# Kernel optimization log

Measured on AMD Instinct MI355X. Metric: run time of the kernel, lower is better.

Reference implementation:

```python
import jax, jax.numpy as jnp
import numpy as np
from jax import lax

KSIZE = 11
SIGMA = 1.5
C1 = (0.01 * 1.0) ** 2
C2 = (0.03 * 1.0) ** 2
PAD = (KSIZE - 1) // 2  # 5


def _gaussian_2d(ksize: int, sigma: float) -> np.ndarray:
    half = (ksize - 1) * 0.5
    g = np.exp(-0.5 * (np.linspace(-half, half, ksize) / sigma) ** 2)
    g = g / g.sum()
    return np.outer(g, g).astype(np.float32)  # [k, k]


def setup_inputs() -> dict:
    key = jax.random.key(0)
    kx, ky = jax.random.split(key)
    B, C, T, H, W = 2, 3, 8, 512, 512
    x = jax.random.uniform(kx, (B, C, T, H, W), dtype=jnp.float32)
    y = jax.random.uniform(ky, (B, C, T, H, W), dtype=jnp.float32)
    k2d = jnp.asarray(_gaussian_2d(KSIZE, SIGMA))
    # depthwise conv3d kernel: [C_out=C, C_in/groups=1, kD=1, kH, kW]
    kernel = jnp.broadcast_to(k2d[None, None, None], (C, 1, 1, KSIZE, KSIZE))
    return {"x": x, "y": y, "kernel": kernel}


def reference(x, y, kernel):
    C = x.shape[1]

    def conv(z):
        return lax.conv_general_dilated(
            z, kernel,
            window_strides=(1, 1, 1),
            padding=((0, 0), (PAD, PAD), (PAD, PAD)),
            dimension_numbers=("NCDHW", "OIDHW", "NCDHW"),
            feature_group_count=C,
        )

    # single grouped conv over the 5 stacked statistics, as in the original
    stacked = jnp.concatenate([x, y, x * x, y * y, x * y], axis=0)
    ux, uy, uxx, uyy, uxy = jnp.split(conv(stacked), 5, axis=0)

    vx = uxx - ux * ux
    vy = uyy - uy * uy
    vxy = uxy - ux * uy
    a1 = 2.0 * ux * uy + C1
    a2 = 2.0 * vxy + C2
    b1 = ux * ux + uy * uy + C1
    b2 = vx + vy + C2
    return a1 * a2 / (b1 * b2)
```

## Files before the change

kernel.cpp:

```cpp
#include <hip/hip_runtime.h>
#include <type_traits>

namespace {
constexpr int HH = 512;
constexpr int WW = 512;
constexpr int KS = 11;
constexpr int PADR = 5;
constexpr int TH = 32;
constexpr int TW = 64;
constexpr int SLAB = 16;
constexpr int HC = TW + 2 * PADR;
constexpr int LP = 80;
constexpr int NTHREADS = 256;
constexpr float SSIM_C1 = 1.0e-4f;
constexpr float SSIM_C2 = 9.0e-4f;
}

__global__ __launch_bounds__(NTHREADS, 4) void ssim_fused(
    const float* __restrict__ x, const float* __restrict__ y,
    const float* __restrict__ kern, float* __restrict__ out)
{
    __shared__ float vb[5][SLAB][LP];

    constexpr int tiles_w = WW / TW;
    constexpr int tiles_h = HH / TH;
    constexpr int tpp = tiles_w * tiles_h;

    const int bid = blockIdx.x;
    const int plane = bid / tpp;
    const int trem = bid - plane * tpp;
    const int tr_idx = trem / tiles_w;
    const int tile_r = tr_idx * TH;
    const int tile_c = (trem - tr_idx * tiles_w) * TW;

    const float* __restrict__ xp = x + (size_t)plane * (HH * WW);
    const float* __restrict__ yp = y + (size_t)plane * (HH * WW);
    float* __restrict__ op = out + (size_t)plane * (HH * WW);

    float wt[KS];
    {
        const float c = kern[5 * KS + 5];
        const float inv = rsqrtf(c);
#pragma unroll
        for (int i = 0; i < KS; ++i) wt[i] = kern[5 * KS + i] * inv;
    }

    const int t = threadIdx.x;
    const bool interior = (tile_r >= PADR) && (tile_r + TH + PADR <= HH) &&
                          (tile_c >= PADR) && (tile_c + TW + PADR <= WW);

    const int p2_r = t >> 4;
    const int p2_c0 = (t & 15) * 4;

    auto run_slab = [&](int s0, auto intr_tag) {
        constexpr bool INTR = decltype(intr_tag)::value;
        for (int i = t; i < (SLAB / 2) * HC; i += NTHREADS) {
            const int r2 = i / HC;
            const int c = i - r2 * HC;
            const int gr = tile_r + s0 + 2 * r2;
            const int gc = tile_c + c - PADR;
            float sxA = 0.f, syA = 0.f, sxxA = 0.f, syyA = 0.f, sxyA = 0.f;
            float sxB = 0.f, syB = 0.f, sxxB = 0.f, syyB = 0.f, sxyB = 0.f;
            if (INTR) {
                const float* xq = xp + (gr - PADR) * WW + gc;
                const float* yq = yp + (gr - PADR) * WW + gc;
#pragma unroll
                for (int k = 0; k < KS + 1; ++k) {
                    const float xv = xq[k * WW];
                    const float yv = yq[k * WW];
                    const float xx = xv * xv;
                    const float yy = yv * yv;
                    const float xy = xv * yv;
                    if (k < KS) {
                        const float w = wt[k];
                        sxA += w * xv;  syA += w * yv;
                        sxxA += w * xx; syyA += w * yy; sxyA += w * xy;
                    }
                    if (k >= 1) {
                        const float w = wt[k - 1];
                        sxB += w * xv;  syB += w * yv;
                        sxxB += w * xx; syyB += w * yy; sxyB += w * xy;
                    }
                }
            } else {
                const bool cok = (gc >= 0) & (gc < WW);
#pragma unroll
                for (int k = 0; k < KS + 1; ++k) {
                    const int rr = gr - PADR + k;
                    const bool ok = cok & (rr >= 0) & (rr < HH);
                    float xv = 0.f, yv = 0.f;
                    if (ok) {
                        xv = xp[rr * WW + gc];
                        yv = yp[rr * WW + gc];
                    }
                    const float xx = xv * xv;
                    const float yy = yv * yv;
                    const float xy = xv * yv;
                    if (k < KS) {
                        const float w = wt[k];
                        sxA += w * xv;  syA += w * yv;
                        sxxA += w * xx; syyA += w * yy; sxyA += w * xy;
                    }
                    if (k >= 1) {
                        const float w = wt[k - 1];
                        sxB += w * xv;  syB += w * yv;
                        sxxB += w * xx; syyB += w * yy; sxyB += w * xy;
                    }
                }
            }
            const int rA = 2 * r2, rB = 2 * r2 + 1;
            vb[0][rA][c] = sxA;   vb[0][rB][c] = sxB;
            vb[1][rA][c] = syA;   vb[1][rB][c] = syB;
            vb[2][rA][c] = sxxA;  vb[2][rB][c] = sxxB;
            vb[3][rA][c] = syyA;  vb[3][rB][c] = syyB;
            vb[4][rA][c] = sxyA;  vb[4][rB][c] = sxyB;
        }
        __syncthreads();

        float res[5][4];
#pragma unroll
        for (int s = 0; s < 5; ++s) {
            const float4 q0 = *(const float4*)&vb[s][p2_r][p2_c0];
            const float4 q1 = *(const float4*)&vb[s][p2_r][p2_c0 + 4];
            const float4 q2 = *(const float4*)&vb[s][p2_r][p2_c0 + 8];
            const float4 q3 = *(const float4*)&vb[s][p2_r][p2_c0 + 12];
            float wnd[16] = {q0.x, q0.y, q0.z, q0.w,
                             q1.x, q1.y, q1.z, q1.w,
                             q2.x, q2.y, q2.z, q2.w,
                             q3.x, q3.y, q3.z, q3.w};
#pragma unroll
            for (int j = 0; j < 4; ++j) {
                float a = 0.f;
#pragma unroll
                for (int k = 0; k < KS; ++k) a += wt[k] * wnd[j + k];
                res[s][j] = a;
            }
        }
        float4 o4;
#pragma unroll
        for (int j = 0; j < 4; ++j) {
            const float ux = res[0][j], uy = res[1][j];
            const float uxx = res[2][j], uyy = res[3][j], uxy = res[4][j];
            const float vx  = uxx - ux * ux;
            const float vy  = uyy - uy * uy;
            const float vxy = uxy - ux * uy;
            const float a1 = 2.f * ux * uy + SSIM_C1;
            const float a2 = 2.f * vxy + SSIM_C2;
            const float b1 = ux * ux + uy * uy + SSIM_C1;
            const float b2 = vx + vy + SSIM_C2;
            (&o4.x)[j] = (a1 * a2) * __builtin_amdgcn_rcpf(b1 * b2);
        }
        *(float4*)(op + (size_t)(tile_r + s0 + p2_r) * WW + (tile_c + p2_c0)) = o4;
        __syncthreads();
    };

    if (interior) {
        run_slab(0,    std::true_type{});
        run_slab(SLAB, std::true_type{});
    } else {
        run_slab(0,    std::false_type{});
        run_slab(SLAB, std::false_type{});
    }
}

extern "C" void kernel_launch(void* const* d_in, const int* in_sizes, int n_in,
                              void* d_out, int out_size, void* d_ws, size_t ws_size,
                              hipStream_t stream) {
    const float* x    = (const float*)d_in[0];
    const float* y    = (const float*)d_in[1];
    const float* kern = (const float*)d_in[2];
    float* out = (float*)d_out;

    const int nplanes = in_sizes[0] / (HH * WW);
    const int nblocks = nplanes * (HH / TH) * (WW / TW);

    ssim_fused<<<dim3(nblocks), dim3(NTHREADS), 0, stream>>>(x, y, kern, out);
}
```

Before: 212.5 us.

## Pack x/y statistics into float2 pairs for packed FMA and interleaved LDS layout

```diff
diff --git a/kernel.cpp b/kernel.cpp
--- a/kernel.cpp
+++ b/kernel.cpp
@@ -10,17 +10,25 @@
 constexpr int TW = 64;
 constexpr int SLAB = 16;
 constexpr int HC = TW + 2 * PADR;
-constexpr int LP = 80;
+constexpr int LPA = 148;
+constexpr int LPC = 76;
 constexpr int NTHREADS = 256;
 constexpr float SSIM_C1 = 1.0e-4f;
 constexpr float SSIM_C2 = 9.0e-4f;
 }
 
+typedef float v2f __attribute__((ext_vector_type(2)));
+typedef float v4f __attribute__((ext_vector_type(4)));
+#define LOWP(v)  __builtin_shufflevector(v, v, 0, 1)
+#define HIGHP(v) __builtin_shufflevector(v, v, 2, 3)
+
 __global__ __launch_bounds__(NTHREADS, 4) void ssim_fused(
     const float* __restrict__ x, const float* __restrict__ y,
     const float* __restrict__ kern, float* __restrict__ out)
 {
-    __shared__ float vb[5][SLAB][LP];
+    __shared__ __align__(16) float pA[SLAB][LPA];
+    __shared__ __align__(16) float pB_[SLAB][LPA];
+    __shared__ __align__(16) float pC_[SLAB][LPC];
 
     constexpr int tiles_w = WW / TW;
     constexpr int tiles_h = HH / TH;
@@ -37,12 +45,15 @@
     const float* __restrict__ yp = y + (size_t)plane * (HH * WW);
     float* __restrict__ op = out + (size_t)plane * (HH * WW);
 
-    float wt[KS];
+    v2f pw[6];
     {
-        const float c = kern[5 * KS + 5];
-        const float inv = rsqrtf(c);
+        const float inv = rsqrtf(kern[5 * KS + 5]);
 #pragma unroll
-        for (int i = 0; i < KS; ++i) wt[i] = kern[5 * KS + i] * inv;
+        for (int i = 0; i < 6; ++i) {
+            const float w = kern[5 * KS + i] * inv;
+            v2f tmp = {w, w};
+            pw[i] = tmp;
+        }
     }
 
     const int t = threadIdx.x;
@@ -50,7 +61,7 @@
                           (tile_c >= PADR) && (tile_c + TW + PADR <= WW);
 
     const int p2_r = t >> 4;
-    const int p2_c0 = (t & 15) * 4;
+    const int p2_m = t & 15;
 
     auto run_slab = [&](int s0, auto intr_tag) {
         constexpr bool INTR = decltype(intr_tag)::value;
@@ -59,99 +70,134 @@
             const int c = i - r2 * HC;
             const int gr = tile_r + s0 + 2 * r2;
             const int gc = tile_c + c - PADR;
-            float sxA = 0.f, syA = 0.f, sxxA = 0.f, syyA = 0.f, sxyA = 0.f;
-            float sxB = 0.f, syB = 0.f, sxxB = 0.f, syyB = 0.f, sxyB = 0.f;
-            if (INTR) {
-                const float* xq = xp + (gr - PADR) * WW + gc;
-                const float* yq = yp + (gr - PADR) * WW + gc;
+            v2f uvA = {0.f, 0.f}, qqA = {0.f, 0.f};
+            v2f uvB = {0.f, 0.f}, qqB = {0.f, 0.f};
+            float xyA = 0.f, xyB = 0.f;
+            const float* xq = xp + (gr - PADR) * WW + gc;
+            const float* yq = yp + (gr - PADR) * WW + gc;
 #pragma unroll
-                for (int k = 0; k < KS + 1; ++k) {
-                    const float xv = xq[k * WW];
-                    const float yv = yq[k * WW];
-                    const float xx = xv * xv;
-                    const float yy = yv * yv;
-                    const float xy = xv * yv;
-                    if (k < KS) {
-                        const float w = wt[k];
-                        sxA += w * xv;  syA += w * yv;
-                        sxxA += w * xx; syyA += w * yy; sxyA += w * xy;
-                    }
-                    if (k >= 1) {
-                        const float w = wt[k - 1];
-                        sxB += w * xv;  syB += w * yv;
-                        sxxB += w * xx; syyB += w * yy; sxyB += w * xy;
-                    }
-                }
-            } else {
-                const bool cok = (gc >= 0) & (gc < WW);
-#pragma unroll
-                for (int k = 0; k < KS + 1; ++k) {
+            for (int k = 0; k < KS + 1; ++k) {
+                float xv, yv;
+                if (INTR) {
+                    xv = xq[k * WW];
+                    yv = yq[k * WW];
+                } else {
                     const int rr = gr - PADR + k;
-                    const bool ok = cok & (rr >= 0) & (rr < HH);
-                    float xv = 0.f, yv = 0.f;
+                    const bool ok = (gc >= 0) & (gc < WW) & (rr >= 0) & (rr < HH);
+                    xv = 0.f; yv = 0.f;
                     if (ok) {
                         xv = xp[rr * WW + gc];
                         yv = yp[rr * WW + gc];
                     }
-                    const float xx = xv * xv;
-                    const float yy = yv * yv;
-                    const float xy = xv * yv;
-                    if (k < KS) {
-                        const float w = wt[k];
-                        sxA += w * xv;  syA += w * yv;
-                        sxxA += w * xx; syyA += w * yy; sxyA += w * xy;
-                    }
-                    if (k >= 1) {
-                        const float w = wt[k - 1];
-                        sxB += w * xv;  syB += w * yv;
-                        sxxB += w * xx; syyB += w * yy; sxyB += w * xy;
-                    }
+                }
+                v2f v2 = {xv, yv};
+                const v2f q2 = v2 * v2;
+                const float xy = xv * yv;
+                if (k < KS) {
+                    const v2f w = pw[k < 6 ? k : 10 - k];
+                    uvA += w * v2;
+                    qqA += w * q2;
+                    xyA += w.x * xy;
+                }
+                if (k >= 1) {
+                    const v2f w = pw[(k - 1) < 6 ? (k - 1) : 11 - k];
+                    uvB += w * v2;
+                    qqB += w * q2;
+                    xyB += w.x * xy;
                 }
             }
             const int rA = 2 * r2, rB = 2 * r2 + 1;
-            vb[0][rA][c] = sxA;   vb[0][rB][c] = sxB;
-            vb[1][rA][c] = syA;   vb[1][rB][c] = syB;
-            vb[2][rA][c] = sxxA;  vb[2][rB][c] = sxxB;
-            vb[3][rA][c] = syyA;  vb[3][rB][c] = syyB;
-            vb[4][rA][c] = sxyA;  vb[4][rB][c] = sxyB;
+            *(v2f*)&pA[rA][2 * c] = uvA;   *(v2f*)&pA[rB][2 * c] = uvB;
+            *(v2f*)&pB_[rA][2 * c] = qqA;  *(v2f*)&pB_[rB][2 * c] = qqB;
+            pC_[rA][c] = xyA;              pC_[rB][c] = xyB;
         }
         __syncthreads();
 
-        float res[5][4];
-#pragma unroll
-        for (int s = 0; s < 5; ++s) {
-            const float4 q0 = *(const float4*)&vb[s][p2_r][p2_c0];
-            const float4 q1 = *(const float4*)&vb[s][p2_r][p2_c0 + 4];
-            const float4 q2 = *(const float4*)&vb[s][p2_r][p2_c0 + 8];
-            const float4 q3 = *(const float4*)&vb[s][p2_r][p2_c0 + 12];
-            float wnd[16] = {q0.x, q0.y, q0.z, q0.w,
-                             q1.x, q1.y, q1.z, q1.w,
-                             q2.x, q2.y, q2.z, q2.w,
-                             q3.x, q3.y, q3.z, q3.w};
-#pragma unroll
-            for (int j = 0; j < 4; ++j) {
-                float a = 0.f;
-#pragma unroll
-                for (int k = 0; k < KS; ++k) a += wt[k] * wnd[j + k];
-                res[s][j] = a;
-            }
-        }
+#define PCONV(R0, R1, R2, R3, a0, a1, a2, a3, a4, a5, a6)                       \
+    R0 += pw[0]*LOWP(a0); R0 += pw[1]*HIGHP(a0); R0 += pw[2]*LOWP(a1);          \
+    R0 += pw[3]*HIGHP(a1); R0 += pw[4]*LOWP(a2); R0 += pw[5]*HIGHP(a2);         \
+    R0 += pw[4]*LOWP(a3); R0 += pw[3]*HIGHP(a3); R0 += pw[2]*LOWP(a4);          \
+    R0 += pw[1]*HIGHP(a4); R0 += pw[0]*LOWP(a5);                                \
+    R1 += pw[0]*HIGHP(a0); R1 += pw[1]*LOWP(a1); R1 += pw[2]*HIGHP(a1);         \
+    R1 += pw[3]*LOWP(a2); R1 += pw[4]*HIGHP(a2); R1 += pw[5]*LOWP(a3);          \
+    R1 += pw[4]*HIGHP(a3); R1 += pw[3]*LOWP(a4); R1 += pw[2]*HIGHP(a4);         \
+    R1 += pw[1]*LOWP(a5); R1 += pw[0]*HIGHP(a5);                                \
+    R2 += pw[0]*LOWP(a1); R2 += pw[1]*HIGHP(a1); R2 += pw[2]*LOWP(a2);          \
+    R2 += pw[3]*HIGHP(a2); R2 += pw[4]*LOWP(a3); R2 += pw[5]*HIGHP(a3);         \
+    R2 += pw[4]*LOWP(a4); R2 += pw[3]*HIGHP(a4); R2 += pw[2]*LOWP(a5);          \
+    R2 += pw[1]*HIGHP(a5); R2 += pw[0]*LOWP(a6);                                \
+    R3 += pw[0]*HIGHP(a1); R3 += pw[1]*LOWP(a2); R3 += pw[2]*HIGHP(a2);         \
+    R3 += pw[3]*LOWP(a3); R3 += pw[4]*HIGHP(a3); R3 += pw[5]*LOWP(a4);          \
+    R3 += pw[4]*HIGHP(a4); R3 += pw[3]*LOWP(a5); R3 += pw[2]*HIGHP(a5);         \
+    R3 += pw[1]*LOWP(a6); R3 += pw[0]*HIGHP(a6);
+
+#define SCONV(R, S0, S1, S2, S3, S4, S5, S6, S7, S8, S9, S10)                   \
+    R += pw[0].x*S0; R += pw[1].x*S1; R += pw[2].x*S2; R += pw[3].x*S3;         \
+    R += pw[4].x*S4; R += pw[5].x*S5; R += pw[4].x*S6; R += pw[3].x*S7;         \
+    R += pw[2].x*S8; R += pw[1].x*S9; R += pw[0].x*S10;
+
+        v2f rUV0 = {0.f, 0.f}, rUV1 = {0.f, 0.f}, rUV2 = {0.f, 0.f}, rUV3 = {0.f, 0.f};
+        {
+            const float* rowA = &pA[p2_r][8 * p2_m];
+            const v4f a0 = *(const v4f*)(rowA + 0);
+            const v4f a1 = *(const v4f*)(rowA + 4);
+            const v4f a2 = *(const v4f*)(rowA + 8);
+            const v4f a3 = *(const v4f*)(rowA + 12);
+            const v4f a4 = *(const v4f*)(rowA + 16);
+            const v4f a5 = *(const v4f*)(rowA + 20);
+            const v4f a6 = *(const v4f*)(rowA + 24);
+            PCONV(rUV0, rUV1, rUV2, rUV3, a0, a1, a2, a3, a4, a5, a6)
+        }
+        v2f rQQ0 = {0.f, 0.f}, rQQ1 = {0.f, 0.f}, rQQ2 = {0.f, 0.f}, rQQ3 = {0.f, 0.f};
+        {
+            const float* rowB = &pB_[p2_r][8 * p2_m];
+            const v4f a0 = *(const v4f*)(rowB + 0);
+            const v4f a1 = *(const v4f*)(rowB + 4);
+            const v4f a2 = *(const v4f*)(rowB + 8);
+            const v4f a3 = *(const v4f*)(rowB + 12);
+            const v4f a4 = *(const v4f*)(rowB + 16);
+            const v4f a5 = *(const v4f*)(rowB + 20);
+            const v4f a6 = *(const v4f*)(rowB + 24);
+            PCONV(rQQ0, rQQ1, rQQ2, rQQ3, a0, a1, a2, a3, a4, a5, a6)
+        }
+        float rC0 = 0.f, rC1 = 0.f, rC2 = 0.f, rC3 = 0.f;
+        {
+            const float* rowC = &pC_[p2_r][4 * p2_m];
+            const v4f c0 = *(const v4f*)(rowC + 0);
+            const v4f c1 = *(const v4f*)(rowC + 4);
+            const v4f c2 = *(const v4f*)(rowC + 8);
+            const v4f c3 = *(const v4f*)(rowC + 12);
+            const float e0 = c0.x, e1 = c0.y, e2 = c0.z, e3 = c0.w;
+            const float e4 = c1.x, e5 = c1.y, e6 = c1.z, e7 = c1.w;
+            const float e8 = c2.x, e9 = c2.y, e10 = c2.z, e11 = c2.w;
+            const float e12 = c3.x, e13 = c3.y;
+            SCONV(rC0, e0, e1, e2, e3, e4, e5, e6, e7, e8, e9, e10)
+            SCONV(rC1, e1, e2, e3, e4, e5, e6, e7, e8, e9, e10, e11)
+            SCONV(rC2, e2, e3, e4, e5, e6, e7, e8, e9, e10, e11, e12)
+            SCONV(rC3, e3, e4, e5, e6, e7, e8, e9, e10, e11, e12, e13)
+        }
+
         float4 o4;
 #pragma unroll
         for (int j = 0; j < 4; ++j) {
-            const float ux = res[0][j], uy = res[1][j];
-            const float uxx = res[2][j], uyy = res[3][j], uxy = res[4][j];
+            const v2f uvj = (j == 0) ? rUV0 : (j == 1) ? rUV1 : (j == 2) ? rUV2 : rUV3;
+            const v2f qqj = (j == 0) ? rQQ0 : (j == 1) ? rQQ1 : (j == 2) ? rQQ2 : rQQ3;
+            const float uxy = (j == 0) ? rC0 : (j == 1) ? rC1 : (j == 2) ? rC2 : rC3;
+            const float ux = uvj.x, uy = uvj.y;
+            const float uxx = qqj.x, uyy = qqj.y;
             const float vx  = uxx - ux * ux;
             const float vy  = uyy - uy * uy;
             const float vxy = uxy - ux * uy;
-            const float a1 = 2.f * ux * uy + SSIM_C1;
-            const float a2 = 2.f * vxy + SSIM_C2;
-            const float b1 = ux * ux + uy * uy + SSIM_C1;
-            const float b2 = vx + vy + SSIM_C2;
-            (&o4.x)[j] = (a1 * a2) * __builtin_amdgcn_rcpf(b1 * b2);
-        }
-        *(float4*)(op + (size_t)(tile_r + s0 + p2_r) * WW + (tile_c + p2_c0)) = o4;
+            const float a1s = 2.f * ux * uy + SSIM_C1;
+            const float a2s = 2.f * vxy + SSIM_C2;
+            const float b1s = ux * ux + uy * uy + SSIM_C1;
+            const float b2s = vx + vy + SSIM_C2;
+            (&o4.x)[j] = (a1s * a2s) * __builtin_amdgcn_rcpf(b1s * b2s);
+        }
+        *(float4*)(op + (size_t)(tile_r + s0 + p2_r) * WW + (tile_c + 4 * p2_m)) = o4;
         __syncthreads();
+#undef PCONV
+#undef SCONV
     };
 
     if (interior) {
```

Measured after the change: 212.5 us. About the same (+0.0%).
